# Kernel tuning notes

Hardware: AMD Instinct MI355X
Metric: run time of the kernel (lower is better)

## Reference

```python
import jax, jax.numpy as jnp
import numpy as np

B, QL, KL, D, H = 2, 2048, 2048, 1024, 16
E = D // H  # head dim


def setup_inputs() -> dict:
    key = jax.random.key(0)
    ks = jax.random.split(key, 12)
    query_features = jax.random.normal(ks[0], (B, QL, D), dtype=jnp.float32)
    key_features = jax.random.normal(ks[1], (B, KL, D), dtype=jnp.float32)
    # causal additive mask [QL, KL]: -inf above the diagonal, 0 elsewhere
    dependency_mask = jnp.where(
        jnp.arange(KL)[None, :] > jnp.arange(QL)[:, None], -jnp.inf, 0.0
    ).astype(jnp.float32)
    # key padding: random valid lengths in [KL//2, KL]; True = padded position
    lengths = jax.random.randint(ks[2], (B,), KL // 2, KL + 1)
    key_padding_mask = jnp.arange(KL)[None, :] >= lengths[:, None]
    s = 0.02
    Wq = jax.random.normal(ks[3], (D, D), jnp.float32) * s
    bq = jax.random.normal(ks[4], (D,), jnp.float32) * s
    Wk = jax.random.normal(ks[5], (D, D), jnp.float32) * s
    bk = jax.random.normal(ks[6], (D,), jnp.float32) * s
    Wv = jax.random.normal(ks[7], (D, D), jnp.float32) * s
    bv = jax.random.normal(ks[8], (D,), jnp.float32) * s
    Wo = jax.random.normal(ks[9], (D, D), jnp.float32) * s
    bo = jax.random.normal(ks[10], (D,), jnp.float32) * s
    return dict(query_features=query_features, key_features=key_features,
                dependency_mask=dependency_mask, key_padding_mask=key_padding_mask,
                Wq=Wq, bq=bq, Wk=Wk, bk=bk, Wv=Wv, bv=bv, Wo=Wo, bo=bo)


def reference(query_features, key_features, dependency_mask, key_padding_mask,
              Wq, bq, Wk, bk, Wv, bv, Wo, bo):
    b, kl, d = key_features.shape
    ql = query_features.shape[1]
    q = query_features @ Wq.T + bq          # [B, QL, D]
    k = key_features @ Wk.T + bk            # [B, KL, D]
    v = key_features @ Wv.T + bv            # [B, KL, D]
    qh = q.reshape(b, ql, H, E)
    kh = k.reshape(b, kl, H, E)
    vh = v.reshape(b, kl, H, E)
    # NOTE: original scales by sqrt(d_model), not sqrt(head_dim)
    scores = jnp.einsum('bqhe,bkhe->bhqk', qh, kh) / jnp.sqrt(jnp.float32(d))
    scores = jnp.where(key_padding_mask[:, None, None, :], -jnp.inf, scores)
    scores = scores + dependency_mask  # broadcast [QL,KL] over [B,H,QL,KL]
    probs = jax.nn.softmax(scores, axis=-1)  # dropout is identity in eval mode
    agg = jnp.einsum('bhqk,bkhe->bqhe', probs, vh).reshape(b, ql, d)
    return agg @ Wo.T + bo
```

## Files before the change

kernel.cpp:

```cpp
#include <hip/hip_runtime.h>
#include <hip/hip_bf16.h>


typedef __bf16 bf16x8 __attribute__((ext_vector_type(8)));
typedef float f32x4 __attribute__((ext_vector_type(4)));
typedef unsigned int u32x4 __attribute__((ext_vector_type(4)));
typedef unsigned short u16;
typedef unsigned int u32;

#define GLOBAL_AS __attribute__((address_space(1)))
#define LDS_AS __attribute__((address_space(3)))

static __device__ __forceinline__ u16 f2bf(float f) {
    __hip_bfloat16 h = __float2bfloat16(f);
    return __builtin_bit_cast(u16, h);
}
static __device__ __forceinline__ u32 pack2bf(float a, float b) {
    return (u32)f2bf(a) | ((u32)f2bf(b) << 16);
}
static __device__ __forceinline__ float exp2_hw(float x) {
    return __builtin_amdgcn_exp2f(x);
}

__global__ void cvt_all(const float* __restrict__ wq_f, const float* __restrict__ wk_f,
                        const float* __restrict__ wv_f, const float* __restrict__ wo_f,
                        u16* __restrict__ wq, u16* __restrict__ wk,
                        u16* __restrict__ wv, u16* __restrict__ wo,
                        const int* __restrict__ kpm, int* __restrict__ lens) {
    int blk = blockIdx.x;
    if (blk >= 4096) {
        const int b = blk - 4096, tid = threadIdx.x;
        int cnt = 0;
        #pragma unroll
        for (int i = 0; i < 8; ++i) cnt += (kpm[b * 2048 + i * 256 + tid] == 0) ? 1 : 0;
        #pragma unroll
        for (int off = 32; off; off >>= 1) cnt += __shfl_down(cnt, off);
        __shared__ int wsum[4];
        if ((tid & 63) == 0) wsum[tid >> 6] = cnt;
        __syncthreads();
        if (tid == 0) lens[b] = wsum[0] + wsum[1] + wsum[2] + wsum[3];
        return;
    }
    int wsel = blk >> 10;
    int i = (blk & 1023) * 256 + threadIdx.x;
    const float* s; u16* d;
    if (wsel == 0)      { s = wq_f; d = wq; }
    else if (wsel == 1) { s = wk_f; d = wk; }
    else if (wsel == 2) { s = wv_f; d = wv; }
    else                { s = wo_f; d = wo; }
    float4 v = reinterpret_cast<const float4*>(s)[i];
    ushort4 o;
    o.x = f2bf(v.x); o.y = f2bf(v.y); o.z = f2bf(v.z); o.w = f2bf(v.w);
    reinterpret_cast<ushort4*>(d)[i] = o;
}

template<int OUT_F32, int BM, int BN>
__device__ __forceinline__
void gemm_body_dbuf(const u16* __restrict__ A, const u16* __restrict__ Bw,
                    const float* __restrict__ bias, void* __restrict__ Cout,
                    int N, int K, float scale, int bx, int by) {
    constexpr int MREP = BM / 32, NREP = BN / 32;
    constexpr int ACH = BM / 8, TCH = ACH + BN / 8;
    constexpr int CPW = TCH / 4;
    __shared__ __attribute__((aligned(16))) u16 aS[2][BM * 64];
    __shared__ __attribute__((aligned(16))) u16 bS[2][BN * 64];
    const int tid = threadIdx.x, wave = tid >> 6, lane = tid & 63;
    const int m0 = by * BM, n0 = bx * BN;
    const int wr = wave >> 1, wc = wave & 1;
    const int fr = lane & 15, fq = lane >> 4;
    const int swz_col = (((lane & 7) ^ (lane >> 3)) * 8);
    const int rsw = (fr & 7) << 3;

    f32x4 acc[MREP][NREP] = {};

    auto stage = [&](int k0, int buf) {
        #pragma unroll
        for (int i = 0; i < CPW; ++i) {
            int chunk = wave * CPW + i;
            const u16* gsrc; u16* ldst;
            if (chunk < ACH) {
                int row = chunk * 8 + (lane >> 3);
                gsrc = A + (size_t)(m0 + row) * K + k0 + swz_col;
                ldst = &aS[buf][chunk * 512];
            } else {
                int row = (chunk - ACH) * 8 + (lane >> 3);
                gsrc = Bw + (size_t)(n0 + row) * K + k0 + swz_col;
                ldst = &bS[buf][(chunk - ACH) * 512];
            }
            __builtin_amdgcn_global_load_lds((GLOBAL_AS void*)gsrc,
                                             (LDS_AS void*)ldst, 16, 0, 0);
        }
    };

    stage(0, 0);
    __syncthreads();
    int cur = 0;

    for (int k0 = 0; k0 < K; k0 += 64) {
        if (k0 + 64 < K) stage(k0 + 64, cur ^ 1);

        bf16x8 af[MREP][2], bfr[NREP][2];
        #pragma unroll
        for (int m = 0; m < MREP; ++m)
            #pragma unroll
            for (int h = 0; h < 2; ++h)
                af[m][h] = *reinterpret_cast<const bf16x8*>(
                    &aS[cur][(wr * (BM / 2) + m * 16 + fr) * 64 + ((h * 32 + fq * 8) ^ rsw)]);
        #pragma unroll
        for (int n = 0; n < NREP; ++n)
            #pragma unroll
            for (int h = 0; h < 2; ++h)
                bfr[n][h] = *reinterpret_cast<const bf16x8*>(
                    &bS[cur][(wc * (BN / 2) + n * 16 + fr) * 64 + ((h * 32 + fq * 8) ^ rsw)]);
        __builtin_amdgcn_s_setprio(1);
        #pragma unroll
        for (int m = 0; m < MREP; ++m)
            #pragma unroll
            for (int n = 0; n < NREP; ++n) {
                acc[m][n] = __builtin_amdgcn_mfma_f32_16x16x32_bf16(af[m][0], bfr[n][0], acc[m][n], 0, 0, 0);
                acc[m][n] = __builtin_amdgcn_mfma_f32_16x16x32_bf16(af[m][1], bfr[n][1], acc[m][n], 0, 0, 0);
            }
        __builtin_amdgcn_s_setprio(0);
        __syncthreads();
        cur ^= 1;
    }

    #pragma unroll
    for (int n = 0; n < NREP; ++n) {
        int col = n0 + wc * (BN / 2) + n * 16 + fr;
        float bv = bias[col];
        #pragma unroll
        for (int m = 0; m < MREP; ++m) {
            #pragma unroll
            for (int j = 0; j < 4; ++j) {
                int row = m0 + wr * (BM / 2) + m * 16 + fq * 4 + j;
                float v = (acc[m][n][j] + bv) * scale;
                if (OUT_F32)
                    reinterpret_cast<float*>(Cout)[(size_t)row * N + col] = v;
                else
                    reinterpret_cast<u16*>(Cout)[(size_t)row * N + col] = f2bf(v);
            }
        }
    }
}

__global__ __launch_bounds__(256, 3)
void gemm_qkv(const float* __restrict__ xq_f, const float* __restrict__ xk_f,
              const u16* __restrict__ wq, const u16* __restrict__ wk,
              const u16* __restrict__ wv,
              const float* __restrict__ bq, const float* __restrict__ bk,
              const float* __restrict__ bv,
              u16* __restrict__ qb, u16* __restrict__ kb, u16* __restrict__ vb) {
    const int id = blockIdx.x;
    const int g = id & 7, s = id >> 3;
    const int z = s >> 5;
    const int xl = (s >> 3) & 3, byl = s & 7;
    const int bx = (g & 1) * 4 + xl;
    const int by = (g >> 1) * 8 + byl;
    const float* Af = (z == 0) ? xq_f : xk_f;
    const u16* W = (z == 0) ? wq : (z == 1) ? wk : wv;
    const float* bias = (z == 0) ? bq : (z == 1) ? bk : bv;
    u16* C = (z == 0) ? qb : (z == 1) ? kb : vb;
    const float scale = (z == 0) ? 0.0450842200f : 1.0f;

    __shared__ __attribute__((aligned(16))) float aSf[128 * 32];
    __shared__ __attribute__((aligned(16))) u16 bS[128 * 32];
    const int tid = threadIdx.x, wave = tid >> 6, lane = tid & 63;
    const int m0 = by * 128, n0 = bx * 128;
    const int wr = wave >> 1, wc = wave & 1;
    const int fr = lane & 15, fq = lane >> 4;
    const int a_sub = lane >> 3, a_g = lane & 7;
    const int b_sub = lane >> 2, b_g = lane & 3;

    f32x4 acc[4][4] = {};

    for (int k0 = 0; k0 < 1024; k0 += 32) {
        #pragma unroll
        for (int i = 0; i < 6; ++i) {
            int chunk = wave * 6 + i;
            if (chunk < 16) {
                int row = chunk * 8 + a_sub;
                const float* gsrc = Af + (size_t)(m0 + row) * 1024 + k0 + ((a_g ^ (row & 7)) * 4);
                __builtin_amdgcn_global_load_lds((GLOBAL_AS void*)gsrc,
                    (LDS_AS void*)(aSf + chunk * 256 + lane * 4), 16, 0, 0);
            } else {
                int bc = chunk - 16;
                int row = bc * 16 + b_sub;
                const u16* gsrc = W + (size_t)(n0 + row) * 1024 + k0 + ((b_g ^ ((row >> 2) & 3)) * 8);
                __builtin_amdgcn_global_load_lds((GLOBAL_AS void*)gsrc,
                    (LDS_AS void*)(bS + bc * 512 + lane * 8), 16, 0, 0);
            }
        }
        __syncthreads();

        bf16x8 af[4];
        #pragma unroll
        for (int m = 0; m < 4; ++m) {
            int row = wr * 64 + m * 16 + fr;
            int r7 = row & 7;
            f32x4 a0 = *reinterpret_cast<const f32x4*>(&aSf[row * 32 + (((2 * fq) ^ r7) * 4)]);
            f32x4 a1 = *reinterpret_cast<const f32x4*>(&aSf[row * 32 + (((2 * fq + 1) ^ r7) * 4)]);
            u32x4 w;
            w[0] = pack2bf(a0[0], a0[1]); w[1] = pack2bf(a0[2], a0[3]);
            w[2] = pack2bf(a1[0], a1[1]); w[3] = pack2bf(a1[2], a1[3]);
            af[m] = __builtin_bit_cast(bf16x8, w);
        }
        bf16x8 bfr[4];
        #pragma unroll
        for (int n = 0; n < 4; ++n) {
            int row = wc * 64 + n * 16 + fr;
            bfr[n] = *reinterpret_cast<const bf16x8*>(
                &bS[row * 32 + ((fq ^ ((row >> 2) & 3)) * 8)]);
        }
        __builtin_amdgcn_s_setprio(1);
        #pragma unroll
        for (int m = 0; m < 4; ++m)
            #pragma unroll
            for (int n = 0; n < 4; ++n)
                acc[m][n] = __builtin_amdgcn_mfma_f32_16x16x32_bf16(af[m], bfr[n], acc[m][n], 0, 0, 0);
        __builtin_amdgcn_s_setprio(0);
        __syncthreads();
    }

    #pragma unroll
    for (int n = 0; n < 4; ++n) {
        int col = n0 + wc * 64 + n * 16 + fr;
        float bv = bias[col];
        #pragma unroll
        for (int m = 0; m < 4; ++m) {
            #pragma unroll
            for (int j = 0; j < 4; ++j) {
                int row = m0 + wr * 64 + m * 16 + fq * 4 + j;
                float v = (acc[m][n][j] + bv) * scale;
                C[(size_t)row * 1024 + col] = f2bf(v);
            }
        }
    }
}

__global__ __launch_bounds__(256, 2)
void gemm_out(const u16* __restrict__ A, const u16* __restrict__ Bw,
              const float* __restrict__ bias, float* __restrict__ Cout) {
    const int id = blockIdx.x;
    const int g = id & 7, s = id >> 3;
    const int xl = s & 3, byl = s >> 2;
    const int bx = (g & 1) * 4 + xl;
    const int by = (g >> 1) * 16 + byl;
    gemm_body_dbuf<1, 64, 128>(A, Bw, bias, Cout, 1024, 1024, 1.0f, bx, by);
}

__global__ __launch_bounds__(256, 4)
void attn_fwd(const u16* __restrict__ Qb, const u16* __restrict__ Kb,
              const u16* __restrict__ Vb, const int* __restrict__ lens,
              u16* __restrict__ Ob) {
    __shared__ __attribute__((aligned(16))) u16 Ks[2][64 * 64];
    __shared__ __attribute__((aligned(16))) u16 Vts[2][64 * 64];
    const int tid = threadIdx.x, wave = tid >> 6, lane = tid & 63;
    const int id = blockIdx.x;
    const int bh = (id & 7) * 4 + ((id >> 3) & 3);
    const int k5 = id >> 5;
    const int g = k5 >> 3, x8 = k5 & 7;
    const int qt = (g == 0) ? x8 : (g == 1) ? 31 - x8 : (g == 2) ? 16 + x8 : 15 - x8;
    const int b = bh >> 4, h = bh & 15;
    const int fr = lane & 15, fq = lane >> 4;
    const int t = wave >> 1;
    const int u = wave & 1;
    const int qbase = qt * 64 + u * 32;
    const int len = lens[b];
    const int nt = min(qt + 1, (len + 63) >> 6);

    bf16x8 qa[2][2];
    #pragma unroll
    for (int gq = 0; gq < 2; ++gq) {
        const size_t qoff = (size_t)(b * 2048 + qbase + gq * 16 + fr) * 1024 + h * 64 + fq * 8;
        qa[gq][0] = *reinterpret_cast<const bf16x8*>(Qb + qoff);
        qa[gq][1] = *reinterpret_cast<const bf16x8*>(Qb + qoff + 32);
    }

    bf16x8 ones;
    #pragma unroll
    for (int i = 0; i < 8; ++i) ones[i] = __builtin_bit_cast(__bf16, (u16)0x3F80);

    f32x4 o_acc[2][4] = {};
    f32x4 lacc[2] = {};

    const int e8 = tid >> 5;
    const int c2 = tid & 31;
    const int kp = 2 * c2;
    const int vhalf = kp >> 5, r5 = kp & 31;
    const int fqv = r5 >> 3, nv = (r5 >> 2) & 1, jv = r5 & 3;
    const int k_src = vhalf * 32 + nv * 16 + fqv * 4 + jv;
    const int kswz_col = (((lane & 7) ^ (lane >> 3)) * 8);

    auto issue_K = [&](int kt, int buf) {
        #pragma unroll
        for (int i = 0; i < 2; ++i) {
            int chunk = wave * 2 + i;
            int krow = chunk * 8 + (lane >> 3);
            const u16* gk = Kb + (size_t)(b * 2048 + kt * 64 + krow) * 1024 + h * 64 + kswz_col;
            __builtin_amdgcn_global_load_lds((GLOBAL_AS void*)gk,
                                             (LDS_AS void*)(&Ks[buf][chunk * 512]), 16, 0, 0);
        }
    };
    auto load_V = [&](int kt, ushort4* r) {
        const u16* b1 = Vb + (size_t)(b * 2048 + kt * 64 + k_src) * 1024 + h * 64 + e8 * 8;
        r[0] = reinterpret_cast<const ushort4*>(b1)[0];
        r[1] = reinterpret_cast<const ushort4*>(b1 + 4)[0];
        r[2] = reinterpret_cast<const ushort4*>(b1 + 1024)[0];
        r[3] = reinterpret_cast<const ushort4*>(b1 + 1024 + 4)[0];
    };
    auto write_V = [&](const ushort4* r, int buf) {
        u32* vbase = reinterpret_cast<u32*>(&Vts[buf][0]);
        const u16* lo16 = reinterpret_cast<const u16*>(&r[0]);
        const u16* hi16 = reinterpret_cast<const u16*>(&r[2]);
        #pragma unroll
        for (int i = 0; i < 8; ++i) {
            u32 w = (u32)lo16[i] | ((u32)hi16[i] << 16);
            vbase[(e8 * 8 + i) * 32 + (c2 ^ (i << 2))] = w;
        }
    };

    {
        ushort4 vr[4];
        issue_K(0, 0);
        load_V(0, vr);
        write_V(vr, 0);
    }
    __syncthreads();

    for (int kt = 0; kt < nt; ++kt) {
        const int k0 = kt * 64;
        const int kbase = k0 + t * 32;
        const int cur = kt & 1, nxt = cur ^ 1;
        const bool has_next = (kt + 1 < nt);

        ushort4 vr[4];
        if (has_next) {
            issue_K(kt + 1, nxt);
            load_V(kt + 1, vr);
        }

        f32x4 s[2][2] = {};
        __builtin_amdgcn_s_setprio(1);
        #pragma unroll
        for (int kq2 = 0; kq2 < 2; ++kq2) {
            int kr = t * 32 + kq2 * 16 + fr;
            int sw = (fr & 7) << 3;
            bf16x8 kb0 = *reinterpret_cast<const bf16x8*>(&Ks[cur][kr * 64 + ((fq * 8) ^ sw)]);
            bf16x8 kb1 = *reinterpret_cast<const bf16x8*>(&Ks[cur][kr * 64 + ((32 + fq * 8) ^ sw)]);
            #pragma unroll
            for (int gq = 0; gq < 2; ++gq) {
                s[kq2][gq] = __builtin_amdgcn_mfma_f32_16x16x32_bf16(kb0, qa[gq][0], s[kq2][gq], 0, 0, 0);
                s[kq2][gq] = __builtin_amdgcn_mfma_f32_16x16x32_bf16(kb1, qa[gq][1], s[kq2][gq], 0, 0, 0);
            }
        }
        __builtin_amdgcn_s_setprio(0);

        const bool fullt = (kbase + 31 <= qbase) && (kbase + 32 <= len);
        if (!fullt) {
            #pragma unroll
            for (int kq2 = 0; kq2 < 2; ++kq2)
                #pragma unroll
                for (int gq = 0; gq < 2; ++gq) {
                    int qg = qbase + gq * 16 + fr;
                    #pragma unroll
                    for (int j = 0; j < 4; ++j) {
                        int kg = kbase + kq2 * 16 + fq * 4 + j;
                        s[kq2][gq][j] = (kg <= qg && kg < len) ? s[kq2][gq][j] : -1e30f;
                    }
                }
        }
        #pragma unroll
        for (int kq2 = 0; kq2 < 2; ++kq2)
            #pragma unroll
            for (int gq = 0; gq < 2; ++gq)
                #pragma unroll
                for (int j = 0; j < 4; ++j)
                    s[kq2][gq][j] = exp2_hw(s[kq2][gq][j]);

        bf16x8 pa[2];
        #pragma unroll
        for (int gq = 0; gq < 2; ++gq) {
            u32x4 w;
            w[0] = pack2bf(s[0][gq][0], s[0][gq][1]);
            w[1] = pack2bf(s[0][gq][2], s[0][gq][3]);
            w[2] = pack2bf(s[1][gq][0], s[1][gq][1]);
            w[3] = pack2bf(s[1][gq][2], s[1][gq][3]);
            pa[gq] = __builtin_bit_cast(bf16x8, w);
        }

        if (has_next) write_V(vr, nxt);

        __builtin_amdgcn_s_setprio(1);
        bf16x8 vbr[4];
        #pragma unroll
        for (int n = 0; n < 4; ++n) {
            int vr2 = n * 16 + fr;
            vbr[n] = *reinterpret_cast<const bf16x8*>(
                &Vts[cur][vr2 * 64 + ((t * 32 + fq * 8) ^ ((fr & 7) << 3))]);
        }
        #pragma unroll
        for (int gq = 0; gq < 2; ++gq) {
            lacc[gq] = __builtin_amdgcn_mfma_f32_16x16x32_bf16(pa[gq], ones, lacc[gq], 0, 0, 0);
            #pragma unroll
            for (int n = 0; n < 4; ++n)
                o_acc[gq][n] = __builtin_amdgcn_mfma_f32_16x16x32_bf16(pa[gq], vbr[n], o_acc[gq][n], 0, 0, 0);
        }
        __builtin_amdgcn_s_setprio(0);

        __syncthreads();
    }

    __syncthreads();
    float* ocomb = reinterpret_cast<float*>(&Ks[0][0]);
    float* lcomb = ocomb + 64 * 68;
    if (t == 1) {
        #pragma unroll
        for (int gq = 0; gq < 2; ++gq)
            #pragma unroll
            for (int j = 0; j < 4; ++j) {
                int ql = u * 32 + gq * 16 + fq * 4 + j;
                #pragma unroll
                for (int n = 0; n < 4; ++n)
                    ocomb[ql * 68 + n * 16 + fr] = o_acc[gq][n][j];
                if (fr == 0) lcomb[ql] = lacc[gq][j];
            }
    }
    __syncthreads();
    if (t == 0) {
        #pragma unroll
        for (int gq = 0; gq < 2; ++gq)
            #pragma unroll
            for (int j = 0; j < 4; ++j) {
                int ql = u * 32 + gq * 16 + fq * 4 + j;
                float inv = 1.f / (lacc[gq][j] + lcomb[ql]);
                int row = qt * 64 + ql;
                #pragma unroll
                for (int n = 0; n < 4; ++n) {
                    float osum = o_acc[gq][n][j] + ocomb[ql * 68 + n * 16 + fr];
                    Ob[(size_t)(b * 2048 + row) * 1024 + h * 64 + n * 16 + fr] = f2bf(osum * inv);
                }
            }
    }
}

extern "C" void kernel_launch(void* const* d_in, const int* in_sizes, int n_in,
                              void* d_out, int out_size, void* d_ws, size_t ws_size,
                              hipStream_t stream) {
    const float* xq_f = (const float*)d_in[0];
    const float* xk_f = (const float*)d_in[1];
    const int* kpm = (const int*)d_in[3];
    const float* Wq = (const float*)d_in[4];
    const float* bq = (const float*)d_in[5];
    const float* Wk = (const float*)d_in[6];
    const float* bk = (const float*)d_in[7];
    const float* Wv = (const float*)d_in[8];
    const float* bv = (const float*)d_in[9];
    const float* Wo = (const float*)d_in[10];
    const float* bo = (const float*)d_in[11];

    u16* ws = (u16*)d_ws;
    u16* xq = ws;
    u16* xk = xq + 4194304;
    u16* wq = xk + 4194304;
    u16* wk = wq + 1048576;
    u16* wv = wk + 1048576;
    u16* wo = wv + 1048576;
    u16* qb = wo + 1048576;
    u16* kb2 = qb + 4194304;
    u16* vb2 = kb2 + 4194304;
    u16* ag = vb2 + 4194304;
    int* lens = (int*)(ag + 4194304);

    cvt_all<<<4098, 256, 0, stream>>>(Wq, Wk, Wv, Wo, wq, wk, wv, wo, kpm, lens);

    gemm_qkv<<<768, 256, 0, stream>>>(xq_f, xk_f, wq, wk, wv,
                                      bq, bk, bv, qb, kb2, vb2);

    attn_fwd<<<1024, 256, 0, stream>>>(qb, kb2, vb2, lens, ag);

    gemm_out<<<512, 256, 0, stream>>>(ag, wo, bo, (float*)d_out);
}
```

Baseline: 106.1 us.

## Pre-convert activations to bf16 and double-buffer the QKV GEMM LDS pipeline

The query and key activations are now converted to bf16 in the conversion kernel alongside the weights, so the QKV projection GEMM loads bf16 activations instead of fp32 ones and converting them inside the inner loop. The GEMM body is rewritten to double-buffer LDS, prefetching the next K-slice while MFMAs run on the current one, with one barrier per iteration. This cuts activation bytes per GEMM tile and overlaps loads with compute. The cost is an extra pass over the activations (fp32 read plus bf16 write) and twice the LDS per block, which may lower occupancy.

Result: faster. 102.8 us (-3.1%).

```diff
diff --git a/kernel.cpp b/kernel.cpp
--- a/kernel.cpp
+++ b/kernel.cpp
@@ -22,14 +22,16 @@
     return __builtin_amdgcn_exp2f(x);
 }
 
-__global__ void cvt_all(const float* __restrict__ wq_f, const float* __restrict__ wk_f,
+__global__ void cvt_all(const float* __restrict__ xq_f, const float* __restrict__ xk_f,
+                        const float* __restrict__ wq_f, const float* __restrict__ wk_f,
                         const float* __restrict__ wv_f, const float* __restrict__ wo_f,
+                        u16* __restrict__ xq, u16* __restrict__ xk,
                         u16* __restrict__ wq, u16* __restrict__ wk,
                         u16* __restrict__ wv, u16* __restrict__ wo,
                         const int* __restrict__ kpm, int* __restrict__ lens) {
     int blk = blockIdx.x;
-    if (blk >= 4096) {
-        const int b = blk - 4096, tid = threadIdx.x;
+    if (blk >= 12288) {
+        const int b = blk - 12288, tid = threadIdx.x;
         int cnt = 0;
         #pragma unroll
         for (int i = 0; i < 8; ++i) cnt += (kpm[b * 2048 + i * 256 + tid] == 0) ? 1 : 0;
@@ -41,17 +43,98 @@
         if (tid == 0) lens[b] = wsum[0] + wsum[1] + wsum[2] + wsum[3];
         return;
     }
-    int wsel = blk >> 10;
-    int i = (blk & 1023) * 256 + threadIdx.x;
-    const float* s; u16* d;
-    if (wsel == 0)      { s = wq_f; d = wq; }
-    else if (wsel == 1) { s = wk_f; d = wk; }
-    else if (wsel == 2) { s = wv_f; d = wv; }
-    else                { s = wo_f; d = wo; }
+    const float* s; u16* d; int i;
+    if (blk < 4096)      { s = xq_f; d = xq; i = blk * 256 + threadIdx.x; }
+    else if (blk < 8192) { s = xk_f; d = xk; i = (blk - 4096) * 256 + threadIdx.x; }
+    else {
+        int wsel = (blk - 8192) >> 10;
+        i = ((blk - 8192) & 1023) * 256 + threadIdx.x;
+        if (wsel == 0)      { s = wq_f; d = wq; }
+        else if (wsel == 1) { s = wk_f; d = wk; }
+        else if (wsel == 2) { s = wv_f; d = wv; }
+        else                { s = wo_f; d = wo; }
+    }
     float4 v = reinterpret_cast<const float4*>(s)[i];
     ushort4 o;
     o.x = f2bf(v.x); o.y = f2bf(v.y); o.z = f2bf(v.z); o.w = f2bf(v.w);
     reinterpret_cast<ushort4*>(d)[i] = o;
+}
+
+__device__ __forceinline__
+void gemm_qkv_body(const u16* __restrict__ A, const u16* __restrict__ Bw,
+                   const float* __restrict__ bias, u16* __restrict__ Cout,
+                   float scale, int bx, int by) {
+    __shared__ __attribute__((aligned(16))) u16 aS[2][128 * 32];
+    __shared__ __attribute__((aligned(16))) u16 bS[2][128 * 32];
+    const int tid = threadIdx.x, wave = tid >> 6, lane = tid & 63;
+    const int m0 = by * 128, n0 = bx * 128;
+    const int wr = wave >> 1, wc = wave & 1;
+    const int fr = lane & 15, fq = lane >> 4;
+    const int crow = lane >> 2;
+    const int sgr = ((lane & 3) ^ (crow & 3)) * 8;
+    const int rg = (fq ^ (fr & 3)) * 8;
+
+    f32x4 acc[4][4] = {};
+
+    auto stage = [&](int k0, int buf) {
+        #pragma unroll
+        for (int i = 0; i < 4; ++i) {
+            int chunk = wave * 4 + i;
+            if (chunk < 8) {
+                int row = chunk * 16 + crow;
+                const u16* gsrc = A + (size_t)(m0 + row) * 1024 + k0 + sgr;
+                __builtin_amdgcn_global_load_lds((GLOBAL_AS void*)gsrc,
+                    (LDS_AS void*)(&aS[buf][chunk * 512 + lane * 8]), 16, 0, 0);
+            } else {
+                int row = (chunk - 8) * 16 + crow;
+                const u16* gsrc = Bw + (size_t)(n0 + row) * 1024 + k0 + sgr;
+                __builtin_amdgcn_global_load_lds((GLOBAL_AS void*)gsrc,
+                    (LDS_AS void*)(&bS[buf][(chunk - 8) * 512 + lane * 8]), 16, 0, 0);
+            }
+        }
+    };
+
+    stage(0, 0);
+    __syncthreads();
+    int cur = 0;
+
+    for (int k0 = 0; k0 < 1024; k0 += 32) {
+        if (k0 + 32 < 1024) stage(k0 + 32, cur ^ 1);
+
+        bf16x8 af[4], bfr[4];
+        #pragma unroll
+        for (int m = 0; m < 4; ++m)
+            af[m] = *reinterpret_cast<const bf16x8*>(
+                &aS[cur][(wr * 64 + m * 16 + fr) * 32 + rg]);
+        #pragma unroll
+        for (int n = 0; n < 4; ++n)
+            bfr[n] = *reinterpret_cast<const bf16x8*>(
+                &bS[cur][(wc * 64 + n * 16 + fr) * 32 + rg]);
+        __builtin_amdgcn_s_setprio(1);
+        #pragma unroll
+        for (int m = 0; m < 4; ++m)
+            #pragma unroll
+            for (int n = 0; n < 4; ++n)
+                acc[m][n] = __builtin_amdgcn_mfma_f32_16x16x32_bf16(af[m], bfr[n], acc[m][n], 0, 0, 0);
+        __builtin_amdgcn_s_setprio(0);
+        __syncthreads();
+        cur ^= 1;
+    }
+
+    #pragma unroll
+    for (int n = 0; n < 4; ++n) {
+        int col = n0 + wc * 64 + n * 16 + fr;
+        float bv = bias[col];
+        #pragma unroll
+        for (int m = 0; m < 4; ++m) {
+            #pragma unroll
+            for (int j = 0; j < 4; ++j) {
+                int row = m0 + wr * 64 + m * 16 + fq * 4 + j;
+                float v = (acc[m][n][j] + bv) * scale;
+                Cout[(size_t)row * 1024 + col] = f2bf(v);
+            }
+        }
+    }
 }
 
 template<int OUT_F32, int BM, int BN>
@@ -145,7 +228,7 @@
 }
 
 __global__ __launch_bounds__(256, 3)
-void gemm_qkv(const float* __restrict__ xq_f, const float* __restrict__ xk_f,
+void gemm_qkv(const u16* __restrict__ xq, const u16* __restrict__ xk,
               const u16* __restrict__ wq, const u16* __restrict__ wk,
               const u16* __restrict__ wv,
               const float* __restrict__ bq, const float* __restrict__ bk,
@@ -157,85 +240,12 @@
     const int xl = (s >> 3) & 3, byl = s & 7;
     const int bx = (g & 1) * 4 + xl;
     const int by = (g >> 1) * 8 + byl;
-    const float* Af = (z == 0) ? xq_f : xk_f;
+    const u16* A = (z == 0) ? xq : xk;
     const u16* W = (z == 0) ? wq : (z == 1) ? wk : wv;
     const float* bias = (z == 0) ? bq : (z == 1) ? bk : bv;
     u16* C = (z == 0) ? qb : (z == 1) ? kb : vb;
     const float scale = (z == 0) ? 0.0450842200f : 1.0f;
-
-    __shared__ __attribute__((aligned(16))) float aSf[128 * 32];
-    __shared__ __attribute__((aligned(16))) u16 bS[128 * 32];
-    const int tid = threadIdx.x, wave = tid >> 6, lane = tid & 63;
-    const int m0 = by * 128, n0 = bx * 128;
-    const int wr = wave >> 1, wc = wave & 1;
-    const int fr = lane & 15, fq = lane >> 4;
-    const int a_sub = lane >> 3, a_g = lane & 7;
-    const int b_sub = lane >> 2, b_g = lane & 3;
-
-    f32x4 acc[4][4] = {};
-
-    for (int k0 = 0; k0 < 1024; k0 += 32) {
-        #pragma unroll
-        for (int i = 0; i < 6; ++i) {
-            int chunk = wave * 6 + i;
-            if (chunk < 16) {
-                int row = chunk * 8 + a_sub;
-                const float* gsrc = Af + (size_t)(m0 + row) * 1024 + k0 + ((a_g ^ (row & 7)) * 4);
-                __builtin_amdgcn_global_load_lds((GLOBAL_AS void*)gsrc,
-                    (LDS_AS void*)(aSf + chunk * 256 + lane * 4), 16, 0, 0);
-            } else {
-                int bc = chunk - 16;
-                int row = bc * 16 + b_sub;
-                const u16* gsrc = W + (size_t)(n0 + row) * 1024 + k0 + ((b_g ^ ((row >> 2) & 3)) * 8);
-                __builtin_amdgcn_global_load_lds((GLOBAL_AS void*)gsrc,
-                    (LDS_AS void*)(bS + bc * 512 + lane * 8), 16, 0, 0);
-            }
-        }
-        __syncthreads();
-
-        bf16x8 af[4];
-        #pragma unroll
-        for (int m = 0; m < 4; ++m) {
-            int row = wr * 64 + m * 16 + fr;
-            int r7 = row & 7;
-            f32x4 a0 = *reinterpret_cast<const f32x4*>(&aSf[row * 32 + (((2 * fq) ^ r7) * 4)]);
-            f32x4 a1 = *reinterpret_cast<const f32x4*>(&aSf[row * 32 + (((2 * fq + 1) ^ r7) * 4)]);
-            u32x4 w;
-            w[0] = pack2bf(a0[0], a0[1]); w[1] = pack2bf(a0[2], a0[3]);
-            w[2] = pack2bf(a1[0], a1[1]); w[3] = pack2bf(a1[2], a1[3]);
-            af[m] = __builtin_bit_cast(bf16x8, w);
-        }
-        bf16x8 bfr[4];
-        #pragma unroll
-        for (int n = 0; n < 4; ++n) {
-            int row = wc * 64 + n * 16 + fr;
-            bfr[n] = *reinterpret_cast<const bf16x8*>(
-                &bS[row * 32 + ((fq ^ ((row >> 2) & 3)) * 8)]);
-        }
-        __builtin_amdgcn_s_setprio(1);
-        #pragma unroll
-        for (int m = 0; m < 4; ++m)
-            #pragma unroll
-            for (int n = 0; n < 4; ++n)
-                acc[m][n] = __builtin_amdgcn_mfma_f32_16x16x32_bf16(af[m], bfr[n], acc[m][n], 0, 0, 0);
-        __builtin_amdgcn_s_setprio(0);
-        __syncthreads();
-    }
-
-    #pragma unroll
-    for (int n = 0; n < 4; ++n) {
-        int col = n0 + wc * 64 + n * 16 + fr;
-        float bv = bias[col];
-        #pragma unroll
-        for (int m = 0; m < 4; ++m) {
-            #pragma unroll
-            for (int j = 0; j < 4; ++j) {
-                int row = m0 + wr * 64 + m * 16 + fq * 4 + j;
-                float v = (acc[m][n][j] + bv) * scale;
-                C[(size_t)row * 1024 + col] = f2bf(v);
-            }
-        }
-    }
+    gemm_qkv_body(A, W, bias, C, scale, bx, by);
 }
 
 __global__ __launch_bounds__(256, 2)
@@ -472,9 +482,10 @@
     u16* ag = vb2 + 4194304;
     int* lens = (int*)(ag + 4194304);
 
-    cvt_all<<<4098, 256, 0, stream>>>(Wq, Wk, Wv, Wo, wq, wk, wv, wo, kpm, lens);
-
-    gemm_qkv<<<768, 256, 0, stream>>>(xq_f, xk_f, wq, wk, wv,
+    cvt_all<<<12290, 256, 0, stream>>>(xq_f, xk_f, Wq, Wk, Wv, Wo,
+                                       xq, xk, wq, wk, wv, wo, kpm, lens);
+
+    gemm_qkv<<<768, 256, 0, stream>>>(xq, xk, wq, wk, wv,
                                       bq, bk, bv, qb, kb2, vb2);
 
     attn_fwd<<<1024, 256, 0, stream>>>(qb, kb2, vb2, lens, ag);
```
